# Kernel optimization log

Measured on AMD Instinct MI355X. Metric: run time of the kernel, lower is better.

Reference implementation:

```python
import jax, jax.numpy as jnp
import numpy as np

B = 8192          # batch
IN = 4096         # in_features
OUT = 4096        # out_features
BS = 64           # block_size
NBR = OUT // BS   # block rows = 64
NBC = IN // BS    # block cols = 64
BPR = 16


def setup_inputs() -> dict:
    key = jax.random.key(0)
    k1, k2, k3 = jax.random.split(key, 3)
    x = jax.random.normal(k1, (B, IN), dtype=jnp.float32)
    values = jax.random.normal(k2, (NBR * BPR, BS, BS), dtype=jnp.float32) * 0.02
    bias = jax.random.normal(k3, (OUT,), dtype=jnp.float32) * 0.02
    # static BSR pattern: per block-row, BPR sorted unique block-column indices
    rng = np.random.default_rng(0)
    cols = np.stack([np.sort(rng.choice(NBC, BPR, replace=False)) for _ in range(NBR)])
    col_indices = jnp.asarray(cols.reshape(-1), dtype=jnp.int32)  # [NBR*BPR]
    return {"x": x, "values": values, "bias": bias, "col_indices": col_indices}


def reference(x, values, bias, col_indices):
    # y = (A_bsr @ x.T).T + bias  ==  x @ A.T + bias, with A in BSR layout.
    xb = x.reshape(B, NBC, BS)                       # [B, nbc, bs] block columns of x
    cols = col_indices.reshape(NBR, BPR)             # [nbr, j]
    xg = xb[:, cols, :]                              # [B, nbr, j, bs] gathered input blocks
    vals = values.reshape(NBR, BPR, BS, BS)          # [nbr, j, bs_out, bs_in]
    out = jnp.einsum('rjob,Brjb->Bro', vals, xg)     # block-sparse GEMM
    return out.reshape(B, OUT) + bias
```

## Files before the change

### kernel.cpp

```cpp
#include <hip/hip_runtime.h>
#include <hip/hip_bf16.h>
#include <stdint.h>

#define B_DIM   8192
#define IN_DIM  4096
#define OUT_DIM 4096
#define BSZ     64
#define NBR_    64
#define BPR_    16
#define KTOT    1024
#define MT      256
#define BKK     32
#define NSTEP   (KTOT / BKK)

typedef __attribute__((ext_vector_type(4))) float  floatx4;
typedef __attribute__((ext_vector_type(8))) short  shortx8;
typedef __attribute__((ext_vector_type(4))) float  fragc;

static __device__ __forceinline__ unsigned short f2bf(float f) {
  __bf16 b = (__bf16)f;
  return __builtin_bit_cast(unsigned short, b);
}

__device__ __forceinline__ void gload_lds16(const void* g, void* l) {
  __builtin_amdgcn_global_load_lds(
      (const __attribute__((address_space(1))) unsigned int*)g,
      (__attribute__((address_space(3))) unsigned int*)l, 16, 0, 0);
}

__global__ __launch_bounds__(256)
void cvt2_kernel(const float* __restrict__ x, const float* __restrict__ v,
                 unsigned short* __restrict__ xb, unsigned short* __restrict__ vb,
                 int xn8, int tn8) {
  const int stride = gridDim.x * blockDim.x;
  for (int i = blockIdx.x * blockDim.x + threadIdx.x; i < tn8; i += stride) {
    const float* src; unsigned short* dst; int idx;
    if (i < xn8) { src = x; dst = xb; idx = i; }
    else         { src = v; dst = vb; idx = i - xn8; }
    floatx4 a = ((const floatx4*)src)[2 * idx];
    floatx4 b = ((const floatx4*)src)[2 * idx + 1];
    uint4 o;
    o.x = (unsigned int)f2bf(a.x) | ((unsigned int)f2bf(a.y) << 16);
    o.y = (unsigned int)f2bf(a.z) | ((unsigned int)f2bf(a.w) << 16);
    o.z = (unsigned int)f2bf(b.x) | ((unsigned int)f2bf(b.y) << 16);
    o.w = (unsigned int)f2bf(b.z) | ((unsigned int)f2bf(b.w) << 16);
    ((uint4*)dst)[idx] = o;
  }
}

__global__ __launch_bounds__(256, 2)
void bsr_gemm(const unsigned short* __restrict__ xb,
              const unsigned short* __restrict__ vb,
              const float* __restrict__ bias, const int* __restrict__ colidx,
              float* __restrict__ out) {
  const int bid  = blockIdx.x;
  const int xcd  = bid & 7;
  const int slot = bid >> 3;
  const int r    = slot & 63;
  const int mt   = xcd * 4 + (slot >> 6);
  const int m0   = mt * MT;

  const int tid  = threadIdx.x;
  const int wave = tid >> 6;
  const int lane = tid & 63;
  const int l16  = lane & 15;
  const int quad = lane >> 4;
  const int sub  = lane >> 2;
  const int slt  = lane & 3;
  const int gsw  = slt ^ ((sub >> 1) & 3);
  const int csw  = quad ^ ((l16 >> 1) & 3);

  __shared__ __align__(16) unsigned short As0[MT * BKK];
  __shared__ __align__(16) unsigned short As1[MT * BKK];
  __shared__ __align__(16) unsigned short As2[MT * BKK];
  __shared__ __align__(16) unsigned short As3[MT * BKK];
  __shared__ __align__(16) unsigned short Bs0[BSZ * BKK];
  __shared__ __align__(16) unsigned short Bs1[BSZ * BKK];
  __shared__ __align__(16) unsigned short Bs2[BSZ * BKK];
  __shared__ __align__(16) unsigned short Bs3[BSZ * BKK];

  int cidx[BPR_];
  #pragma unroll
  for (int j = 0; j < BPR_; ++j)
    cidx[j] = __builtin_amdgcn_readfirstlane(colidx[r * BPR_ + j]);

  const unsigned short* gA =
      xb + (size_t)(m0 + wave * 64 + sub) * IN_DIM + gsw * 8;
  const unsigned short* gB =
      vb + ((size_t)(r * BPR_) * BSZ + wave * 16 + sub) * BSZ + gsw * 8;

  const int aoff = (wave * 64 + l16) * BKK + csw * 8;
  const int boff = l16 * BKK + csw * 8;

  fragc acc[4][4] = {};

#define STAGE(k, As, Bs)                                                      \
  {                                                                           \
    const int jb_ = (k) >> 1, kb0_ = ((k) & 1) * BKK;                         \
    const int colo_ = cidx[jb_] * BSZ + kb0_;                                 \
    _Pragma("unroll")                                                         \
    for (int i_ = 0; i_ < 4; ++i_)                                            \
      gload_lds16(gA + (size_t)i_ * 16 * IN_DIM + colo_,                      \
                  &As[(wave * 64 + i_ * 16) * BKK]);                          \
    gload_lds16(gB + (size_t)jb_ * BSZ * BSZ + kb0_,                          \
                &Bs[(wave * 16) * BKK]);                                      \
  }

#define COMP(As, Bs)                                                          \
  {                                                                           \
    shortx8 af_[4], bf_[4];                                                   \
    _Pragma("unroll")                                                         \
    for (int mi = 0; mi < 4; ++mi)                                            \
      af_[mi] = *(const shortx8*)&As[aoff + mi * 16 * BKK];                   \
    _Pragma("unroll")                                                         \
    for (int ni = 0; ni < 4; ++ni)                                            \
      bf_[ni] = *(const shortx8*)&Bs[boff + ni * 16 * BKK];                   \
    _Pragma("unroll")                                                         \
    for (int mi = 0; mi < 4; ++mi) {                                          \
      _Pragma("unroll")                                                       \
      for (int ni = 0; ni < 4; ++ni)                                          \
        acc[mi][ni] = __builtin_amdgcn_mfma_f32_16x16x32_bf16(                \
            af_[mi], bf_[ni], acc[mi][ni], 0, 0, 0);                          \
    }                                                                         \
  }

#define ITER(k, Ac, Bc, An, Bn)                                              \
  do {                                                                       \
    if ((k) < NSTEP - 2)                                                     \
      asm volatile("s_waitcnt vmcnt(10)" ::: "memory");                      \
    else if ((k) == NSTEP - 2)                                               \
      asm volatile("s_waitcnt vmcnt(5)" ::: "memory");                       \
    else                                                                     \
      asm volatile("s_waitcnt vmcnt(0)" ::: "memory");                       \
    __builtin_amdgcn_s_barrier();                                            \
    asm volatile("" ::: "memory");                                           \
    if ((k) + 3 < NSTEP) { STAGE((k) + 3, An, Bn); }                         \
    COMP(Ac, Bc);                                                            \
  } while (0)

  STAGE(0, As0, Bs0);
  STAGE(1, As1, Bs1);
  STAGE(2, As2, Bs2);

  #pragma unroll
  for (int k = 0; k < NSTEP; k += 4) {
    ITER(k + 0, As0, Bs0, As3, Bs3);
    ITER(k + 1, As1, Bs1, As0, Bs0);
    ITER(k + 2, As2, Bs2, As1, Bs1);
    ITER(k + 3, As3, Bs3, As2, Bs2);
  }
#undef STAGE
#undef COMP
#undef ITER

  #pragma unroll
  for (int ni = 0; ni < 4; ++ni) {
    const int col = r * BSZ + ni * 16 + l16;
    const float bv = bias[col];
    #pragma unroll
    for (int mi = 0; mi < 4; ++mi) {
      #pragma unroll
      for (int reg = 0; reg < 4; ++reg) {
        const int row = m0 + wave * 64 + mi * 16 + quad * 4 + reg;
        out[(size_t)row * OUT_DIM + col] = acc[mi][ni][reg] + bv;
      }
    }
  }
}

__global__ __launch_bounds__(256)
void bsr_naive(const float* __restrict__ x, const float* __restrict__ v,
               const float* __restrict__ bias, const int* __restrict__ colidx,
               float* __restrict__ out) {
  const size_t gid = (size_t)blockIdx.x * blockDim.x + threadIdx.x;
  if (gid >= (size_t)B_DIM * OUT_DIM) return;
  const int b = gid / OUT_DIM;
  const int oc = gid % OUT_DIM;
  const int rr = oc / BSZ, o = oc % BSZ;
  float s = bias[oc];
  for (int j = 0; j < BPR_; ++j) {
    const int c = colidx[rr * BPR_ + j];
    const float* xp = x + (size_t)b * IN_DIM + c * BSZ;
    const float* vp = v + ((size_t)(rr * BPR_ + j) * BSZ + o) * BSZ;
    for (int k = 0; k < BSZ; ++k) s += vp[k] * xp[k];
  }
  out[gid] = s;
}

extern "C" void kernel_launch(void* const* d_in, const int* in_sizes, int n_in,
                              void* d_out, int out_size, void* d_ws, size_t ws_size,
                              hipStream_t stream) {
  const float* x    = (const float*)d_in[0];
  const float* vals = (const float*)d_in[1];
  const float* bias = (const float*)d_in[2];
  const int*   cols = (const int*)d_in[3];
  float* out = (float*)d_out;

  const size_t x_elems = (size_t)B_DIM * IN_DIM;
  const size_t v_elems = (size_t)NBR_ * BPR_ * BSZ * BSZ;
  const size_t xb_bytes = x_elems * sizeof(unsigned short);
  const size_t vb_bytes = v_elems * sizeof(unsigned short);

  if (ws_size >= xb_bytes + vb_bytes) {
    unsigned short* xbp = (unsigned short*)d_ws;
    unsigned short* vbp = (unsigned short*)((char*)d_ws + xb_bytes);
    const int xn8 = (int)(x_elems / 8);
    const int tn8 = (int)((x_elems + v_elems) / 8);
    cvt2_kernel<<<dim3(9216), dim3(256), 0, stream>>>(x, vals, xbp, vbp, xn8, tn8);
    bsr_gemm<<<dim3(NBR_ * (B_DIM / MT)), dim3(256), 0, stream>>>(
        xbp, vbp, bias, cols, out);
  } else {
    const size_t n = (size_t)B_DIM * OUT_DIM;
    bsr_naive<<<dim3((unsigned)((n + 255) / 256)), dim3(256), 0, stream>>>(
        x, vals, bias, cols, out);
  }
}
```

Measured before the change: 338.3 us.

## Fuse fp32-to-bf16 conversion of x into GEMM LDS fragment loads

Drops the separate pass that converted the whole x matrix to bf16 in workspace. The GEMM now streams fp32 x tiles directly into LDS with a new XOR swizzle and packs them to bf16 when building MFMA fragments. Only the weight values are still pre-converted. To keep the fp32 tiles within the same LDS budget, the M tile is halved from 256 to 128, so there are twice as many blocks and each block reads the B tile twice as often relative to its work. Each x element is also converted once per block-row that touches it rather than once overall.

```diff
diff --git a/kernel.cpp b/kernel.cpp
--- a/kernel.cpp
+++ b/kernel.cpp
@@ -9,7 +9,7 @@
 #define NBR_    64
 #define BPR_    16
 #define KTOT    1024
-#define MT      256
+#define MT      128
 #define BKK     32
 #define NSTEP   (KTOT / BKK)
 
@@ -20,6 +20,15 @@
 static __device__ __forceinline__ unsigned short f2bf(float f) {
   __bf16 b = (__bf16)f;
   return __builtin_bit_cast(unsigned short, b);
+}
+
+static __device__ __forceinline__ shortx8 pack8(floatx4 a, floatx4 b) {
+  shortx8 p;
+  p[0] = (short)f2bf(a[0]); p[1] = (short)f2bf(a[1]);
+  p[2] = (short)f2bf(a[2]); p[3] = (short)f2bf(a[3]);
+  p[4] = (short)f2bf(b[0]); p[5] = (short)f2bf(b[1]);
+  p[6] = (short)f2bf(b[2]); p[7] = (short)f2bf(b[3]);
+  return p;
 }
 
 __device__ __forceinline__ void gload_lds16(const void* g, void* l) {
@@ -29,27 +38,21 @@
 }
 
 __global__ __launch_bounds__(256)
-void cvt2_kernel(const float* __restrict__ x, const float* __restrict__ v,
-                 unsigned short* __restrict__ xb, unsigned short* __restrict__ vb,
-                 int xn8, int tn8) {
-  const int stride = gridDim.x * blockDim.x;
-  for (int i = blockIdx.x * blockDim.x + threadIdx.x; i < tn8; i += stride) {
-    const float* src; unsigned short* dst; int idx;
-    if (i < xn8) { src = x; dst = xb; idx = i; }
-    else         { src = v; dst = vb; idx = i - xn8; }
-    floatx4 a = ((const floatx4*)src)[2 * idx];
-    floatx4 b = ((const floatx4*)src)[2 * idx + 1];
-    uint4 o;
-    o.x = (unsigned int)f2bf(a.x) | ((unsigned int)f2bf(a.y) << 16);
-    o.y = (unsigned int)f2bf(a.z) | ((unsigned int)f2bf(a.w) << 16);
-    o.z = (unsigned int)f2bf(b.x) | ((unsigned int)f2bf(b.y) << 16);
-    o.w = (unsigned int)f2bf(b.z) | ((unsigned int)f2bf(b.w) << 16);
-    ((uint4*)dst)[idx] = o;
-  }
+void cvt_v(const float* __restrict__ v, unsigned short* __restrict__ vb, int n8) {
+  const int idx = blockIdx.x * 256 + threadIdx.x;
+  if (idx >= n8) return;
+  floatx4 a = ((const floatx4*)v)[2 * idx];
+  floatx4 b = ((const floatx4*)v)[2 * idx + 1];
+  uint4 o;
+  o.x = (unsigned int)f2bf(a.x) | ((unsigned int)f2bf(a.y) << 16);
+  o.y = (unsigned int)f2bf(a.z) | ((unsigned int)f2bf(a.w) << 16);
+  o.z = (unsigned int)f2bf(b.x) | ((unsigned int)f2bf(b.y) << 16);
+  o.w = (unsigned int)f2bf(b.z) | ((unsigned int)f2bf(b.w) << 16);
+  ((uint4*)vb)[idx] = o;
 }
 
 __global__ __launch_bounds__(256, 2)
-void bsr_gemm(const unsigned short* __restrict__ xb,
+void bsr_gemm(const float* __restrict__ x,
               const unsigned short* __restrict__ vb,
               const float* __restrict__ bias, const int* __restrict__ colidx,
               float* __restrict__ out) {
@@ -57,7 +60,7 @@
   const int xcd  = bid & 7;
   const int slot = bid >> 3;
   const int r    = slot & 63;
-  const int mt   = xcd * 4 + (slot >> 6);
+  const int mt   = xcd * 8 + (slot >> 6);
   const int m0   = mt * MT;
 
   const int tid  = threadIdx.x;
@@ -69,11 +72,15 @@
   const int slt  = lane & 3;
   const int gsw  = slt ^ ((sub >> 1) & 3);
   const int csw  = quad ^ ((l16 >> 1) & 3);
-
-  __shared__ __align__(16) unsigned short As0[MT * BKK];
-  __shared__ __align__(16) unsigned short As1[MT * BKK];
-  __shared__ __align__(16) unsigned short As2[MT * BKK];
-  __shared__ __align__(16) unsigned short As3[MT * BKK];
+  const int sub8 = lane >> 3;
+  const int slt8 = lane & 7;
+  const int gsw8 = slt8 ^ sub8;
+  const int s0   = (2 * quad) ^ (l16 & 7);
+
+  __shared__ __align__(16) float          As0[MT * BKK];
+  __shared__ __align__(16) float          As1[MT * BKK];
+  __shared__ __align__(16) float          As2[MT * BKK];
+  __shared__ __align__(16) float          As3[MT * BKK];
   __shared__ __align__(16) unsigned short Bs0[BSZ * BKK];
   __shared__ __align__(16) unsigned short Bs1[BSZ * BKK];
   __shared__ __align__(16) unsigned short Bs2[BSZ * BKK];
@@ -84,15 +91,14 @@
   for (int j = 0; j < BPR_; ++j)
     cidx[j] = __builtin_amdgcn_readfirstlane(colidx[r * BPR_ + j]);
 
-  const unsigned short* gA =
-      xb + (size_t)(m0 + wave * 64 + sub) * IN_DIM + gsw * 8;
+  const float* gA =
+      x + (size_t)(m0 + wave * 32 + sub8) * IN_DIM + gsw8 * 4;
   const unsigned short* gB =
       vb + ((size_t)(r * BPR_) * BSZ + wave * 16 + sub) * BSZ + gsw * 8;
 
-  const int aoff = (wave * 64 + l16) * BKK + csw * 8;
   const int boff = l16 * BKK + csw * 8;
 
-  fragc acc[4][4] = {};
+  fragc acc[2][4] = {};
 
 #define STAGE(k, As, Bs)                                                      \
   {                                                                           \
@@ -100,23 +106,27 @@
     const int colo_ = cidx[jb_] * BSZ + kb0_;                                 \
     _Pragma("unroll")                                                         \
     for (int i_ = 0; i_ < 4; ++i_)                                            \
-      gload_lds16(gA + (size_t)i_ * 16 * IN_DIM + colo_,                      \
-                  &As[(wave * 64 + i_ * 16) * BKK]);                          \
+      gload_lds16(gA + (size_t)i_ * 8 * IN_DIM + colo_,                       \
+                  &As[(wave * 32 + i_ * 8) * BKK]);                           \
     gload_lds16(gB + (size_t)jb_ * BSZ * BSZ + kb0_,                          \
                 &Bs[(wave * 16) * BKK]);                                      \
   }
 
 #define COMP(As, Bs)                                                          \
   {                                                                           \
-    shortx8 af_[4], bf_[4];                                                   \
-    _Pragma("unroll")                                                         \
-    for (int mi = 0; mi < 4; ++mi)                                            \
-      af_[mi] = *(const shortx8*)&As[aoff + mi * 16 * BKK];                   \
+    shortx8 af_[2], bf_[4];                                                   \
+    _Pragma("unroll")                                                         \
+    for (int mi = 0; mi < 2; ++mi) {                                          \
+      const float* ap_ = &As[(wave * 32 + mi * 16 + l16) * BKK];              \
+      floatx4 a0_ = *(const floatx4*)(ap_ + s0 * 4);                          \
+      floatx4 a1_ = *(const floatx4*)(ap_ + (s0 ^ 1) * 4);                    \
+      af_[mi] = pack8(a0_, a1_);                                              \
+    }                                                                         \
     _Pragma("unroll")                                                         \
     for (int ni = 0; ni < 4; ++ni)                                            \
       bf_[ni] = *(const shortx8*)&Bs[boff + ni * 16 * BKK];                   \
     _Pragma("unroll")                                                         \
-    for (int mi = 0; mi < 4; ++mi) {                                          \
+    for (int mi = 0; mi < 2; ++mi) {                                          \
       _Pragma("unroll")                                                       \
       for (int ni = 0; ni < 4; ++ni)                                          \
         acc[mi][ni] = __builtin_amdgcn_mfma_f32_16x16x32_bf16(                \
@@ -158,10 +168,10 @@
     const int col = r * BSZ + ni * 16 + l16;
     const float bv = bias[col];
     #pragma unroll
-    for (int mi = 0; mi < 4; ++mi) {
+    for (int mi = 0; mi < 2; ++mi) {
       #pragma unroll
       for (int reg = 0; reg < 4; ++reg) {
-        const int row = m0 + wave * 64 + mi * 16 + quad * 4 + reg;
+        const int row = m0 + wave * 32 + mi * 16 + quad * 4 + reg;
         out[(size_t)row * OUT_DIM + col] = acc[mi][ni][reg] + bv;
       }
     }
@@ -196,19 +206,16 @@
   const int*   cols = (const int*)d_in[3];
   float* out = (float*)d_out;
 
-  const size_t x_elems = (size_t)B_DIM * IN_DIM;
-  const size_t v_elems = (size_t)NBR_ * BPR_ * BSZ * BSZ;
-  const size_t xb_bytes = x_elems * sizeof(unsigned short);
+  const size_t v_elems  = (size_t)NBR_ * BPR_ * BSZ * BSZ;
   const size_t vb_bytes = v_elems * sizeof(unsigned short);
 
-  if (ws_size >= xb_bytes + vb_bytes) {
-    unsigned short* xbp = (unsigned short*)d_ws;
-    unsigned short* vbp = (unsigned short*)((char*)d_ws + xb_bytes);
-    const int xn8 = (int)(x_elems / 8);
-    const int tn8 = (int)((x_elems + v_elems) / 8);
-    cvt2_kernel<<<dim3(9216), dim3(256), 0, stream>>>(x, vals, xbp, vbp, xn8, tn8);
+  if (ws_size >= vb_bytes) {
+    unsigned short* vbp = (unsigned short*)d_ws;
+    const int n8 = (int)(v_elems / 8);
+    cvt_v<<<dim3((unsigned)((n8 + 255) / 256)), dim3(256), 0, stream>>>(
+        vals, vbp, n8);
     bsr_gemm<<<dim3(NBR_ * (B_DIM / MT)), dim3(256), 0, stream>>>(
-        xbp, vbp, bias, cols, out);
+        x, vbp, bias, cols, out);
   } else {
     const size_t n = (size_t)B_DIM * OUT_DIM;
     bsr_naive<<<dim3((unsigned)((n + 255) / 256)), dim3(256), 0, stream>>>(
```

Result: slower. 379.7 us (+12.2%).
